# Optimization experiments

Measured on AMD Instinct MI355X. Metric: run time of the kernel, lower is better.

The kernel has to match this reference:

```python
import jax, jax.numpy as jnp
import numpy as np
from jax import lax

V, E, H, B, P, Q = 50000, 300, 256, 32, 400, 40


def _cell(x, h, c, Wih, Whh, b):
    # torch nn.LSTMCell math (b = b_ih + b_hh), gate order i,f,g,o
    g = x @ Wih.T + h @ Whh.T + b
    i, f, gg, o = jnp.split(g, 4, axis=-1)
    c2 = jax.nn.sigmoid(f) * c + jax.nn.sigmoid(i) * jnp.tanh(gg)
    return jax.nn.sigmoid(o) * jnp.tanh(c2), c2


def setup_inputs():
    key = jax.random.key(0)
    ks = jax.random.split(key, 26)
    n = lambda k, s: jax.random.normal(k, s, jnp.float32) * 0.05
    return {
        "passage_ids": jax.random.randint(ks[0], (P, B), 0, V),
        "question_ids": jax.random.randint(ks[1], (Q, B), 0, V),
        "passage_lens": jax.random.randint(ks[2], (B,), P // 2, P + 1),
        "question_lens": jax.random.randint(ks[3], (B,), Q // 2, Q + 1),
        "answer": jax.random.randint(ks[4], (2, B), 0, P // 2),
        "embed": n(ks[5], (V, E)),
        "pre_Wih": n(ks[6], (4 * H, E)),
        "pre_Whh": n(ks[7], (4 * H, H)),
        "pre_b": n(ks[8], (4 * H,)),
        "Wq": n(ks[9], (H, H)),
        "Wp": n(ks[10], (H, H)),
        "bp": n(ks[11], (H,)),
        "Wh": n(ks[12], (H, H)),
        "w_alpha": n(ks[13], (H,)),
        "b_alpha": n(ks[14], ()),
        "m_Wih": n(ks[15], (4 * H, 2 * H)),
        "m_Whh": n(ks[16], (4 * H, H)),
        "m_b": n(ks[17], (4 * H,)),
        "Wm": n(ks[18], (2 * H, H)),
        "Wa": n(ks[19], (H, H)),
        "ba": n(ks[20], (H,)),
        "w_beta": n(ks[21], (H,)),
        "b_beta": n(ks[22], ()),
        "p_Wih": n(ks[23], (4 * H, 2 * H)),
        "p_Whh": n(ks[24], (4 * H, H)),
        "p_b": n(ks[25], (4 * H,)),
    }


def _forward(embed, pre_Wih, pre_Whh, pre_b, Wq, Wp, bp, Wh, w_alpha, b_alpha,
             m_Wih, m_Whh, m_b, Wm, Wa, ba, w_beta, b_beta, p_Wih, p_Whh, p_b,
             passage_ids, passage_lens, question_ids, question_lens):
    Hd = pre_Whh.shape[1]
    Bd = passage_ids.shape[1]
    z0 = jnp.zeros((Bd, Hd), jnp.float32)

    def preprocess(ids, lens):
        x = embed[ids]                                       # [T,B,E]
        T = x.shape[0]
        m = (jnp.arange(T)[:, None] < lens[None, :]).astype(jnp.float32)[:, :, None]  # [T,B,1]
        def step(carry, inp):
            h, c = carry
            xt, mt = inp
            _, c2 = _cell(xt, h, c, pre_Wih, pre_Whh, pre_b)
            h2 = jnp.tanh(c2) * mt                           # module quirk: h := tanh(c)
            return (h2, c2 * mt), h2
        _, Hs = lax.scan(step, (z0, z0), (x, m))
        return Hs, m

    Hp, mP = preprocess(passage_ids, passage_lens)           # [P,B,H]
    Hq, _ = preprocess(question_ids, question_lens)          # [Q,B,H]

    attQ = Hq @ Wq                                           # [Q,B,H]

    def match(Hp_dir, m_dir):
        def step(carry, inp):
            h, c = carry
            hp, mt = inp                                     # hp [B,H], mt [B,1]
            g = jnp.tanh(attQ + hp @ Wp + bp + h @ Wh)       # [Q,B,H]
            alpha = jax.nn.softmax(g @ w_alpha + b_alpha, axis=0)  # softmax over question time [Q,B]
            wq = jnp.einsum('qb,qbh->bh', alpha, Hq)
            zt = jnp.concatenate([hp, wq], axis=-1) * mt
            h2, c2 = _cell(zt, h, c, m_Wih, m_Whh, m_b)
            h2 = h2 * mt
            return (h2, c2 * mt), h2
        _, Hs = lax.scan(step, (z0, z0), (Hp_dir, m_dir))
        return Hs

    Hf = match(Hp, mP)
    Hb = match(Hp[::-1], mP[::-1])[::-1]
    Hr = jnp.concatenate([Hf, Hb], axis=-1)                  # [P,B,2H]

    attM = Hr @ Wm                                           # [P,B,H]
    valid = (jnp.arange(Hr.shape[0])[:, None] < passage_lens[None, :]).astype(jnp.float32)  # [P,B]
    ha, ca = z0, z0
    dists = []
    for _ in range(2):                                       # start / end pointer
        Fk = jnp.tanh(attM + ha @ Wa + ba)                   # [P,B,H]
        scores = Fk @ w_beta + b_beta                        # [P,B]
        scores = jnp.where(valid > 0, scores, -1e30)
        beta = jax.nn.softmax(scores, axis=0) * valid        # zeros past passage length, like original
        dists.append(beta.T)                                 # [B,P]
        wHr = jnp.einsum('pb,pbh->bh', beta, Hr)
        ha, ca = _cell(wHr, ha, ca, p_Wih, p_Whh, p_b)
    return jnp.stack(dists)                                  # [2,B,P]


def reference(passage_ids, question_ids, passage_lens, question_lens, answer,
              embed, pre_Wih, pre_Whh, pre_b, Wq, Wp, bp, Wh, w_alpha, b_alpha,
              m_Wih, m_Whh, m_b, Wm, Wa, ba, w_beta, b_beta, p_Wih, p_Whh, p_b):
    # `answer` only feeds the training loss in the original; forward returns the distributions.
    return _forward(embed, pre_Wih, pre_Whh, pre_b, Wq, Wp, bp, Wh, w_alpha, b_alpha,
                    m_Wih, m_Whh, m_b, Wm, Wa, ba, w_beta, b_beta, p_Wih, p_Whh, p_b,
                    passage_ids, passage_lens, question_ids, question_lens)
```

## Files before the change

kernel.cpp:

```cpp
#include <hip/hip_runtime.h>
#include <hip/hip_bf16.h>

typedef __attribute__((ext_vector_type(8))) short short8;
typedef __attribute__((ext_vector_type(4))) float f32x4;
typedef __attribute__((ext_vector_type(2))) float f32x2;
typedef unsigned short u16;
typedef unsigned int u32;

#define DEV __device__ __forceinline__

static constexpr int Hd    = 256;
static constexpr int Bb    = 32;
static constexpr int Pp    = 400;
static constexpr int Qq    = 40;
static constexpr int NROWS = Pp * Bb + Qq * Bb;
static constexpr int PROBE_MAGIC = 1234567;
static constexpr int NPROBE = 14;

DEV float bf2f(u16 u) { u32 i = ((u32)u) << 16; float f; __builtin_memcpy(&f, &i, 4); return f; }
DEV u16 f2bf(float f) { u32 i; __builtin_memcpy(&i, &f, 4); i += 0x7FFFu + ((i >> 16) & 1u); return (u16)(i >> 16); }
DEV float sigf(float x) { return __builtin_amdgcn_rcpf(1.f + __expf(-x)); }
DEV float tanhf_(float x) {
  float ax = __builtin_fabsf(x);
  float t = __expf(2.f * ax);
  float r = 1.f - 2.f * __builtin_amdgcn_rcpf(t + 1.f);
  return x < 0.f ? -r : r;
}
DEV f32x4 mfma32(short8 a, short8 b, f32x4 c) {
  return __builtin_amdgcn_mfma_f32_16x16x32_bf16(a, b, c, 0, 0, 0);
}
DEV short8 zero8() { short8 z = {0,0,0,0,0,0,0,0}; return z; }

struct KArgs {
  const int *pids, *qids, *plen, *qlen;
  const float *embedF, *preWihF, *preWhhF, *preBF, *WqF, *WpF, *bpF, *WhF,
              *walphaF, *balphaF, *mWihF, *mWhhF, *mBF, *WmF, *WaF, *baF,
              *wbetaF, *bbetaF, *pWihF, *pWhhF, *pBF;
  int* bar;
  u16 *WqT, *WpT, *WmT, *WihP, *Xpad, *preX, *Hp, *Hq, *Hrb, *wq, *wHr, *haB,
      *attQb, *pWihB, *pWhhB, *mWxb, *WhTb, *xW;
  float *hpWp, *attM, *scores, *aWa, *gatesW;
  float* out;
};

DEV void probe_mark(int* bar, int idx) {
  if (blockIdx.x == 0 && threadIdx.x == 0)
    __hip_atomic_store(bar + 768 + idx, PROBE_MAGIC, __ATOMIC_RELEASE, __HIP_MEMORY_SCOPE_AGENT);
}

DEV void barn(int* base, int grp, int n, int gen) {
  __syncthreads();
  if (threadIdx.x == 0) {
    int* c = base + grp * 128;
    int* g = base + grp * 128 + 64;
    if (__hip_atomic_fetch_add(c, 1, __ATOMIC_ACQ_REL, __HIP_MEMORY_SCOPE_AGENT) == n - 1) {
      __hip_atomic_store(c, 0, __ATOMIC_RELAXED, __HIP_MEMORY_SCOPE_AGENT);
      __hip_atomic_store(g, gen, __ATOMIC_RELEASE, __HIP_MEMORY_SCOPE_AGENT);
    } else {
      while (__hip_atomic_load(g, __ATOMIC_RELAXED, __HIP_MEMORY_SCOPE_AGENT) < gen)
        __builtin_amdgcn_s_sleep(1);
      __builtin_amdgcn_fence(__ATOMIC_ACQUIRE, "agent");
    }
  }
  __syncthreads();
}

__global__ __launch_bounds__(256) void k_prep(KArgs A) {
  const int gtid = blockIdx.x * 256 + threadIdx.x;
  const int GS = 256 * 256;
  for (int idx = gtid; idx < 1024 * 160; idx += GS) {
    int row = idx / 160, cd = idx - row * 160;
    u32 v = 0;
    if (cd < 150) {
      f32x2 e2 = *(const f32x2*)(A.preWihF + (size_t)row * 300 + cd * 2);
      v = (u32)f2bf(e2[0]) | ((u32)f2bf(e2[1]) << 16);
    }
    *(u32*)(A.WihP + (size_t)row * 320 + cd * 2) = v;
  }
  for (int idx = gtid; idx < NROWS * 160; idx += GS) {
    int row = idx / 160, cd = idx - row * 160;
    int id = (row < Pp * Bb) ? A.pids[row] : A.qids[row - Pp * Bb];
    u32 v = 0;
    if (cd < 150) {
      f32x2 e2 = *(const f32x2*)(A.embedF + (size_t)id * 300 + cd * 2);
      v = (u32)f2bf(e2[0]) | ((u32)f2bf(e2[1]) << 16);
    }
    *(u32*)(A.Xpad + (size_t)row * 320 + cd * 2) = v;
  }
  for (int idx = gtid; idx < 65536; idx += GS) {
    int r = idx >> 8, c = idx & 255;
    A.WqT[idx]  = f2bf(A.WqF[c * 256 + r]);
    A.WpT[idx]  = f2bf(A.WpF[c * 256 + r]);
    A.WhTb[idx] = f2bf(A.WhF[c * 256 + r]);
  }
  for (int idx = gtid; idx < 131072; idx += GS) {
    int r = idx >> 9, c = idx & 511;
    A.WmT[idx] = f2bf(A.WmF[c * 256 + r]);
  }
  for (int idx = gtid; idx < 1024 * 256; idx += GS) {
    int n = idx >> 8, k = idx & 255;
    A.mWxb[idx] = f2bf(A.mWihF[(size_t)n * 512 + k]);
  }
  for (int idx = gtid; idx < 524288 + 262144; idx += GS) {
    if (idx < 524288) A.pWihB[idx] = f2bf(A.pWihF[idx]);
    else              A.pWhhB[idx - 524288] = f2bf(A.pWhhF[idx - 524288]);
  }
  if (gtid < 32 * 256) {
    A.aWa[gtid] = A.baF[gtid & 255];
    A.haB[gtid] = 0;
  }
  probe_mark(A.bar, 0);
}

struct GemmArgs { const u16* Ag; int lda; const u16* Bg; int ldb; int Mt64, Nt64, nk; float* Cf; u16* Cb; int ldc; int* bar; int probe; };

__global__ __launch_bounds__(512) void k_gemm(GemmArgs g) {
  const int tid = threadIdx.x, lane = tid & 63;
  const int r16 = lane & 15, kl = (lane >> 4) * 8;
  const int ntile = g.Mt64 * g.Nt64;
  const int stride = gridDim.x * 8;
  for (int tix = blockIdx.x * 8 + (tid >> 6); tix < ntile; tix += stride) {
    int m0 = (tix / g.Nt64) * 64, n0 = (tix % g.Nt64) * 64;
    f32x4 acc[4][4] = {};
    for (int kb = 0; kb < g.nk; ++kb) {
      int k0 = kb * 32 + kl;
      short8 a[4], b[4];
#pragma unroll
      for (int i = 0; i < 4; ++i) {
        a[i] = *(const short8*)(g.Ag + (size_t)(m0 + i * 16 + r16) * g.lda + k0);
        b[i] = *(const short8*)(g.Bg + (size_t)(n0 + i * 16 + r16) * g.ldb + k0);
      }
#pragma unroll
      for (int mi = 0; mi < 4; ++mi)
#pragma unroll
        for (int ni = 0; ni < 4; ++ni) acc[mi][ni] = mfma32(a[mi], b[ni], acc[mi][ni]);
    }
#pragma unroll
    for (int mi = 0; mi < 4; ++mi)
#pragma unroll
      for (int ni = 0; ni < 4; ++ni)
#pragma unroll
        for (int j = 0; j < 4; ++j) {
          int r = m0 + mi * 16 + (lane >> 4) * 4 + j, cc = n0 + ni * 16 + r16;
          if (g.Cf) g.Cf[(size_t)r * g.ldc + cc] = acc[mi][ni][j];
          else      g.Cb[(size_t)r * g.ldc + cc] = f2bf(acc[mi][ni][j]);
        }
  }
  probe_mark(g.bar, g.probe);
}

__global__ __launch_bounds__(512) void k_prescan(KArgs A) {
  __shared__ __align__(16) unsigned char sm[33280];
  float* PRE = (float*)(sm + 24576);
  float* CL  = (float*)(sm + 30720);
  float* PBL = (float*)(sm + 32768);
  const int blk = blockIdx.x;
  const int gi  = blk & 15;
  const int grp = blk >> 4;
  const int steps  = grp ? Qq : Pp;
  const int* lens  = grp ? A.qlen : A.plen;
  u16* Hs          = grp ? A.Hq : A.Hp;
  const int xoff   = grp ? Pp * Bb : 0;

  const int tid = threadIdx.x, lane = tid & 63, wv = tid >> 6;
  const int r16 = lane & 15, kl = (lane >> 4) * 8;
  const int h0 = gi * 16;

  for (int idx = tid; idx < 48 * 256; idx += 512) {
    int row = idx >> 8, k = idx & 255;
    int gate = (row >> 4) * 256 + h0 + (row & 15);
    int byte = row * 512 + ((2 * k) ^ ((row & 7) << 4));
    *(u16*)(sm + byte) = f2bf(A.preWhhF[(size_t)gate * 256 + k]);
  }
  for (int idx = tid; idx < 32 * 16; idx += 512) CL[idx] = 0.f;
  if (tid < 48) PBL[tid] = A.preBF[(tid >> 4) * 256 + h0 + (tid & 15)];
  __syncthreads();

  int gen = 0;
#pragma unroll 1
  for (int t = 0; t < steps; ++t) {
    if (wv < 6) {
      int mi = wv & 1, ni = wv >> 1;
      int chain = mi * 16 + r16;
      f32x4 acc = {0.f, 0.f, 0.f, 0.f};
#pragma unroll
      for (int kb = 0; kb < 8; ++kb) {
        int k0 = kb * 32 + kl;
        short8 a = zero8();
        if (t > 0) a = *(const short8*)(Hs + (size_t)((t - 1) * 32 + chain) * 256 + k0);
        int row = ni * 16 + r16;
        short8 b = *(const short8*)(sm + row * 512 + ((2 * k0) ^ ((row & 7) << 4)));
        acc = mfma32(a, b, acc);
      }
      int col = ni * 16 + r16;
#pragma unroll
      for (int j = 0; j < 4; ++j)
        PRE[(mi * 16 + (lane >> 4) * 4 + j) * 48 + col] = acc[j];
    }
    __syncthreads();
    {
      int chain = tid >> 4, hd = tid & 15;
      size_t xr = (size_t)(xoff + t * 32 + chain) * 1024;
      float ip = PRE[chain * 48 + hd]      + bf2f(A.preX[xr + h0 + hd])       + PBL[hd];
      float fp = PRE[chain * 48 + 16 + hd] + bf2f(A.preX[xr + 256 + h0 + hd]) + PBL[16 + hd];
      float gp = PRE[chain * 48 + 32 + hd] + bf2f(A.preX[xr + 512 + h0 + hd]) + PBL[32 + hd];
      float c2 = sigf(fp) * CL[chain * 16 + hd] + sigf(ip) * tanhf_(gp);
      float mt = (t < lens[chain]) ? 1.f : 0.f;
      float h2 = tanhf_(c2) * mt;
      c2 *= mt;
      CL[chain * 16 + hd] = c2;
      Hs[(size_t)(t * 32 + chain) * 256 + h0 + hd] = f2bf(h2);
    }
    barn(A.bar, grp, 16, ++gen);
  }
  probe_mark(A.bar, 2);
}

__global__ __launch_bounds__(512) void k_match(KArgs A) {
  __shared__ __align__(16) unsigned char sm[81920];
  float* PRE = (float*)(sm + 65536);
  float* CL  = (float*)(sm + 73728);
  float* EL  = (float*)(sm + 75776);
  float* SL  = (float*)(sm + 77824);
  float* AL  = (float*)(sm + 78336);
  float* BPL = (float*)(sm + 78848);
  float* WAL = (float*)(sm + 79872);
  float* MBL = (float*)(sm + 80896);

  const int blk = blockIdx.x;
  const int gi  = blk & 15;
  const int dir = blk >> 4;
  const int grp = 2 + dir;
  const int tid = threadIdx.x, lane = tid & 63, wv = tid >> 6;
  const int r16 = lane & 15, kl = (lane >> 4) * 8;
  const int h0 = gi * 16;

  for (int idx = tid; idx < 64 * 512; idx += 512) {
    int row = idx >> 9, k = idx & 511;
    int gate = (row >> 4) * 256 + h0 + (row & 15);
    float v = (k < 256) ? A.mWihF[(size_t)gate * 512 + 256 + k]
                        : A.mWhhF[(size_t)gate * 256 + (k - 256)];
    int byte = row * 1024 + ((2 * k) ^ ((row & 7) << 4));
    *(u16*)(sm + byte) = f2bf(v);
  }
  for (int idx = tid; idx < 32 * 16; idx += 512) CL[idx] = 0.f;
  if (tid < 256) { BPL[tid] = A.bpF[tid]; WAL[tid] = A.walphaF[tid]; }
  if (tid < 64) MBL[tid] = A.mBF[(tid >> 4) * 256 + h0 + (tid & 15)];
  __syncthreads();

  const float bAl = A.balphaF[0];
  int gen = 0;
#pragma unroll 1
  for (int t = 0; t < Pp; ++t) {
    int p  = dir ? (Pp - 1 - t) : t;
    int pp = dir ? (p + 1) : (p - 1);
    barn(A.bar, grp, 16, ++gen);

    if (t == 0) {
      EL[tid] = 0.f;
    } else {
      f32x4 acc0 = {0.f,0.f,0.f,0.f}, acc1 = {0.f,0.f,0.f,0.f};
#pragma unroll
      for (int kb = 0; kb < 8; ++kb) {
        int k0 = kb * 32 + kl;
        short8 a = zero8();
        if (r16 < 2)
          a = *(const short8*)(A.Hrb + (size_t)(pp * 32 + gi * 2 + r16) * 512 + dir * 256 + k0);
        short8 bA = *(const short8*)(A.WhTb + (size_t)(wv * 32 + r16) * 256 + k0);
        short8 bB = *(const short8*)(A.WhTb + (size_t)(wv * 32 + 16 + r16) * 256 + k0);
        acc0 = mfma32(a, bA, acc0);
        acc1 = mfma32(a, bB, acc1);
      }
      if ((lane >> 4) == 0) {
        EL[0 * 256 + wv * 32 + r16]      = acc0[0];
        EL[1 * 256 + wv * 32 + r16]      = acc0[1];
        EL[0 * 256 + wv * 32 + 16 + r16] = acc1[0];
        EL[1 * 256 + wv * 32 + 16 + r16] = acc1[1];
      }
    }
    __syncthreads();
    {
      int c = wv >> 2;
      int b = gi * 2 + c;
      float base[4];
#pragma unroll
      for (int j = 0; j < 4; ++j) {
        int h = lane + 64 * j;
        base[j] = A.hpWp[(size_t)(p * 32 + b) * 256 + h] + BPL[h] + EL[c * 256 + h];
      }
      int q4 = wv & 3;
#pragma unroll
      for (int i = 0; i < 10; ++i) {
        int q = q4 + 4 * i;
        float s = 0.f;
#pragma unroll
        for (int j = 0; j < 4; ++j) {
          int h = lane + 64 * j;
          s += WAL[h] * tanhf_(bf2f(A.attQb[(size_t)(q * 32 + b) * 256 + h]) + base[j]);
        }
#pragma unroll
        for (int off = 32; off; off >>= 1) s += __shfl_xor(s, off, 64);
        if (lane == 0) SL[c * 40 + q] = s;
      }
    }
    __syncthreads();
    if ((wv & 3) == 0) {
      int c = wv >> 2;
      float x = (lane < 40) ? (SL[c * 40 + lane] + bAl) : -3.4e38f;
      float m = x;
#pragma unroll
      for (int off = 32; off; off >>= 1) m = fmaxf(m, __shfl_xor(m, off, 64));
      float e = (lane < 40) ? __expf(x - m) : 0.f;
      float su = e;
#pragma unroll
      for (int off = 32; off; off >>= 1) su += __shfl_xor(su, off, 64);
      if (lane < 40) AL[c * 40 + lane] = e / su;
    }
    __syncthreads();
    {
      int c = tid >> 8, h = tid & 255;
      int b = gi * 2 + c;
      float acc = 0.f;
#pragma unroll 8
      for (int q = 0; q < 40; ++q) acc += AL[c * 40 + q] * bf2f(A.Hq[(size_t)(q * 32 + b) * 256 + h]);
      float mt = (p < A.plen[b]) ? 1.f : 0.f;
      A.wq[(size_t)(dir * 32 + b) * 256 + h] = f2bf(acc * mt);
    }
    barn(A.bar, grp, 16, ++gen);

    {
      int mi = wv >> 2, ni = wv & 3;
      int chain = mi * 16 + r16;
      f32x4 acc = {0.f, 0.f, 0.f, 0.f};
#pragma unroll
      for (int kb = 0; kb < 16; ++kb) {
        int k0 = kb * 32 + kl;
        short8 a;
        if (kb < 8) a = *(const short8*)(A.wq + (size_t)(dir * 32 + chain) * 256 + k0);
        else {
          if (t == 0) a = zero8();
          else        a = *(const short8*)(A.Hrb + (size_t)(pp * 32 + chain) * 512 + dir * 256 + (k0 - 256));
        }
        int row = ni * 16 + r16;
        short8 b = *(const short8*)(sm + row * 1024 + ((2 * k0) ^ ((row & 7) << 4)));
        acc = mfma32(a, b, acc);
      }
      int col = ni * 16 + r16;
#pragma unroll
      for (int j = 0; j < 4; ++j)
        PRE[(mi * 16 + (lane >> 4) * 4 + j) * 64 + col] = acc[j];
    }
    __syncthreads();
    {
      int chain = tid >> 4, hd = tid & 15;
      size_t xr = (size_t)(p * 32 + chain) * 1024 + h0 + hd;
      float ig = PRE[chain * 64 + hd]      + MBL[hd]      + bf2f(A.xW[xr]);
      float fg = PRE[chain * 64 + 16 + hd] + MBL[16 + hd] + bf2f(A.xW[xr + 256]);
      float gg = PRE[chain * 64 + 32 + hd] + MBL[32 + hd] + bf2f(A.xW[xr + 512]);
      float og = PRE[chain * 64 + 48 + hd] + MBL[48 + hd] + bf2f(A.xW[xr + 768]);
      float c2 = sigf(fg) * CL[chain * 16 + hd] + sigf(ig) * tanhf_(gg);
      float h2 = sigf(og) * tanhf_(c2);
      float mt = (p < A.plen[chain]) ? 1.f : 0.f;
      c2 *= mt; h2 *= mt;
      CL[chain * 16 + hd] = c2;
      A.Hrb[(size_t)(p * 32 + chain) * 512 + dir * 256 + h0 + hd] = f2bf(h2);
    }
  }
  probe_mark(A.bar, 6);
}

__global__ __launch_bounds__(512) void k_scores(KArgs A, int probe) {
  const int blk = blockIdx.x, tid = threadIdx.x, lane = tid & 63, wv = tid >> 6;
  for (int j = wv; j < 50; j += 8) {
    int id = blk * 50 + j;
    int p = id >> 5, b = id & 31;
    float s = 0.f;
#pragma unroll
    for (int jj = 0; jj < 4; ++jj) {
      int h = lane + 64 * jj;
      s += A.wbetaF[h] * tanhf_(A.attM[(size_t)(p * 32 + b) * 256 + h] + A.aWa[b * 256 + h]);
    }
#pragma unroll
    for (int off = 32; off; off >>= 1) s += __shfl_xor(s, off, 64);
    if (lane == 0)
      A.scores[p * 32 + b] = (p < A.plen[b]) ? (s + A.bbetaF[0]) : -1e30f;
  }
  probe_mark(A.bar, probe);
}

__global__ __launch_bounds__(512) void k_soft(KArgs A, int k, int probe) {
  __shared__ __align__(16) unsigned char sm[2048];
  float* BL = (float*)sm;
  float* RED = (float*)(sm + 1664);
  const int b = blockIdx.x, tid = threadIdx.x, lane = tid & 63, wv = tid >> 6;
  float x = (tid < 400) ? A.scores[tid * 32 + b] : -3.4e38f;
  float m = x;
#pragma unroll
  for (int off = 32; off; off >>= 1) m = fmaxf(m, __shfl_xor(m, off, 64));
  if (lane == 0) RED[wv] = m;
  __syncthreads();
  if (tid == 0) {
    float mm = RED[0];
#pragma unroll
    for (int i = 1; i < 8; ++i) mm = fmaxf(mm, RED[i]);
    RED[0] = mm;
  }
  __syncthreads();
  float M = RED[0];
  float e = (tid < 400) ? __expf(x - M) : 0.f;
  float su = e;
#pragma unroll
  for (int off = 32; off; off >>= 1) su += __shfl_xor(su, off, 64);
  if (lane == 0) RED[8 + wv] = su;
  __syncthreads();
  if (tid == 0) {
    float ss = 0.f;
#pragma unroll
    for (int i = 0; i < 8; ++i) ss += RED[8 + i];
    RED[8] = ss;
  }
  __syncthreads();
  float SUM = RED[8];
  if (tid < 400) {
    float beta = (e / SUM) * ((tid < A.plen[b]) ? 1.f : 0.f);
    A.out[(size_t)(k * 32 + b) * 400 + tid] = beta;
    BL[tid] = beta;
  }
  if (k == 0) {
    __syncthreads();
    float acc = 0.f;
#pragma unroll 4
    for (int p = 0; p < 400; ++p) acc += BL[p] * bf2f(A.Hrb[(size_t)(p * 32 + b) * 512 + tid]);
    A.wHr[b * 512 + tid] = f2bf(acc);
  }
  probe_mark(A.bar, probe);
}

__global__ __launch_bounds__(128) void k_pgates(KArgs A) {
  const int blk = blockIdx.x, tid = threadIdx.x, lane = tid & 63, wv = tid >> 6;
  const int r16 = lane & 15, kl = (lane >> 4) * 8;
  const int g0 = blk * 16;
  const int mi = wv, chain = mi * 16 + r16;
  f32x4 acc = {0.f, 0.f, 0.f, 0.f};
#pragma unroll
  for (int kb = 0; kb < 24; ++kb) {
    int k0 = kb * 32 + kl;
    short8 a, b;
    if (kb < 16) {
      a = *(const short8*)(A.wHr + (size_t)chain * 512 + k0);
      b = *(const short8*)(A.pWihB + (size_t)(g0 + r16) * 512 + k0);
    } else {
      a = *(const short8*)(A.haB + (size_t)chain * 256 + (k0 - 512));
      b = *(const short8*)(A.pWhhB + (size_t)(g0 + r16) * 256 + (k0 - 512));
    }
    acc = mfma32(a, b, acc);
  }
#pragma unroll
  for (int j = 0; j < 4; ++j)
    A.gatesW[(size_t)(mi * 16 + (lane >> 4) * 4 + j) * 1024 + g0 + r16] = acc[j];
  probe_mark(A.bar, 10);
}

__global__ __launch_bounds__(256) void k_pcell(KArgs A) {
  __shared__ float HL[256];
  const int b = blockIdx.x, hd = threadIdx.x;
  {
    float ig = A.gatesW[(size_t)b * 1024 + hd]       + A.pBF[hd];
    float gg = A.gatesW[(size_t)b * 1024 + 512 + hd] + A.pBF[512 + hd];
    float og = A.gatesW[(size_t)b * 1024 + 768 + hd] + A.pBF[768 + hd];
    float c2 = sigf(ig) * tanhf_(gg);
    float h2 = sigf(og) * tanhf_(c2);
    HL[hd] = h2;
    A.haB[b * 256 + hd] = f2bf(h2);
  }
  __syncthreads();
  {
    float acc = A.baF[hd];
#pragma unroll 8
    for (int kk = 0; kk < 256; ++kk) acc += HL[kk] * A.WaF[(size_t)kk * 256 + hd];
    A.aWa[b * 256 + hd] = acc;
  }
  probe_mark(A.bar, 11);
}

__global__ __launch_bounds__(64) void k_diag(KArgs A) {
  if (threadIdx.x == 0 && blockIdx.x == 0) {
    int bad = -1;
    for (int i = 0; i < NPROBE; ++i) {
      int v = __hip_atomic_load(A.bar + 768 + i, __ATOMIC_ACQUIRE, __HIP_MEMORY_SCOPE_AGENT);
      if (v != PROBE_MAGIC) { bad = i; break; }
    }
    if (bad >= 0) {
      float s = 128.f * (float)(1 << bad);
      for (int j = 0; j < 8; ++j) A.out[j] = s;
    }
  }
}

extern "C" void kernel_launch(void* const* d_in, const int* in_sizes, int n_in,
                              void* d_out, int out_size, void* d_ws, size_t ws_size,
                              hipStream_t stream) {
  (void)in_sizes; (void)n_in; (void)ws_size;
  KArgs A;
  A.pids = (const int*)d_in[0];
  A.qids = (const int*)d_in[1];
  A.plen = (const int*)d_in[2];
  A.qlen = (const int*)d_in[3];
  A.embedF  = (const float*)d_in[5];
  A.preWihF = (const float*)d_in[6];
  A.preWhhF = (const float*)d_in[7];
  A.preBF   = (const float*)d_in[8];
  A.WqF     = (const float*)d_in[9];
  A.WpF     = (const float*)d_in[10];
  A.bpF     = (const float*)d_in[11];
  A.WhF     = (const float*)d_in[12];
  A.walphaF = (const float*)d_in[13];
  A.balphaF = (const float*)d_in[14];
  A.mWihF   = (const float*)d_in[15];
  A.mWhhF   = (const float*)d_in[16];
  A.mBF     = (const float*)d_in[17];
  A.WmF     = (const float*)d_in[18];
  A.WaF     = (const float*)d_in[19];
  A.baF     = (const float*)d_in[20];
  A.wbetaF  = (const float*)d_in[21];
  A.bbetaF  = (const float*)d_in[22];
  A.pWihF   = (const float*)d_in[23];
  A.pWhhF   = (const float*)d_in[24];
  A.pBF     = (const float*)d_in[25];

  char* w = (char*)d_ws;
  size_t off = 0;
  auto take = [&](size_t bytes) { void* p = w + off; off += (bytes + 255) & ~(size_t)255; return p; };
  A.bar    = (int*)take(4096);
  A.WqT    = (u16*)take(256 * 256 * 2);
  A.WpT    = (u16*)take(256 * 256 * 2);
  A.WmT    = (u16*)take(256 * 512 * 2);
  A.WihP   = (u16*)take((size_t)1024 * 320 * 2);
  A.Xpad   = (u16*)take((size_t)NROWS * 320 * 2);
  A.preX   = (u16*)take((size_t)NROWS * 1024 * 2);
  A.Hp     = (u16*)take((size_t)Pp * Bb * 256 * 2);
  A.Hq     = (u16*)take((size_t)Qq * Bb * 256 * 2);
  A.Hrb    = (u16*)take((size_t)Pp * Bb * 512 * 2);
  A.wq     = (u16*)take(2 * 32 * 256 * 2);
  A.wHr    = (u16*)take(32 * 512 * 2);
  A.haB    = (u16*)take(32 * 256 * 2);
  A.attQb  = (u16*)take((size_t)Qq * Bb * 256 * 2);
  A.pWihB  = (u16*)take((size_t)1024 * 512 * 2);
  A.pWhhB  = (u16*)take((size_t)1024 * 256 * 2);
  A.mWxb   = (u16*)take((size_t)1024 * 256 * 2);
  A.WhTb   = (u16*)take((size_t)256 * 256 * 2);
  A.hpWp   = (float*)take((size_t)Pp * Bb * 256 * 4);
  A.attM   = (float*)take((size_t)Pp * Bb * 256 * 4);
  A.scores = (float*)take((size_t)Pp * Bb * 4);
  A.aWa    = (float*)take(32 * 256 * 4);
  A.gatesW = (float*)take((size_t)32 * 1024 * 4);
  A.xW     = A.preX;
  A.out    = (float*)d_out;

  hipMemsetAsync(d_out, 0x3C, 64, stream);
  hipMemsetAsync(A.bar, 0, 4096, stream);

  (void)hipGetLastError();
  size_t outB = (size_t)out_size * 4;
  int li = 0;
#define CK  if (hipGetLastError() != hipSuccess) { hipMemsetAsync(d_out, 0x41 + li, outB, stream); return; } ++li;

  hipLaunchKernelGGL(k_prep, dim3(256), dim3(256), 0, stream, A); CK;

  GemmArgs g1{A.Xpad, 320, A.WihP, 320, NROWS / 64, 16, 10, nullptr, A.preX, 1024, A.bar, 1};
  hipLaunchKernelGGL(k_gemm, dim3(256), dim3(512), 0, stream, g1); CK;

  hipLaunchKernelGGL(k_prescan, dim3(32), dim3(512), 0, stream, A); CK;

  GemmArgs g2{A.Hq, 256, A.WqT, 256, 20, 4, 8, nullptr, A.attQb, 256, A.bar, 3};
  hipLaunchKernelGGL(k_gemm, dim3(16), dim3(512), 0, stream, g2); CK;
  GemmArgs g3{A.Hp, 256, A.WpT, 256, 200, 4, 8, A.hpWp, nullptr, 256, A.bar, 4};
  hipLaunchKernelGGL(k_gemm, dim3(128), dim3(512), 0, stream, g3); CK;
  GemmArgs gx{A.Hp, 256, A.mWxb, 256, 200, 16, 8, nullptr, A.xW, 1024, A.bar, 5};
  hipLaunchKernelGGL(k_gemm, dim3(256), dim3(512), 0, stream, gx); CK;

  hipLaunchKernelGGL(k_match, dim3(32), dim3(512), 0, stream, A); CK;

  GemmArgs g4{A.Hrb, 512, A.WmT, 512, 200, 4, 16, A.attM, nullptr, 256, A.bar, 7};
  hipLaunchKernelGGL(k_gemm, dim3(128), dim3(512), 0, stream, g4); CK;

  hipLaunchKernelGGL(k_scores, dim3(256), dim3(512), 0, stream, A, 8); CK;
  hipLaunchKernelGGL(k_soft,   dim3(32),  dim3(512), 0, stream, A, 0, 9); CK;
  hipLaunchKernelGGL(k_pgates, dim3(64),  dim3(128), 0, stream, A); CK;
  hipLaunchKernelGGL(k_pcell,  dim3(32),  dim3(256), 0, stream, A); CK;
  hipLaunchKernelGGL(k_scores, dim3(256), dim3(512), 0, stream, A, 12); CK;
  hipLaunchKernelGGL(k_soft,   dim3(32),  dim3(512), 0, stream, A, 1, 13); CK;

  hipLaunchKernelGGL(k_diag,   dim3(1),   dim3(64),  0, stream, A); CK;
#undef CK
}
```

Before: 9.596 ms.

## Restructure match-LSTM step to prefetch inputs, split Wh projection, overlap GEMM with barrier

Each block now holds its 16-column slice of Wh in shared memory. After computing its h slice, it writes a partial h@Wh product to a per-block global buffer. At the next step the attention term sums the 16 partials instead of running a full 256x256 GEMM over the previous Hr row. Loop-invariant loads (attQ, hpWp, xW, Hq, preX) are hoisted ahead of the grid barrier, and the Hr half of the gate GEMM is issued before the barrier so it overlaps the wait. Global stores and loads of shared recurrent state switch to relaxed atomics with packed 32-bit stores, and the barrier acquire uses an atomic load. The cost is more register pressure, extra shared memory, and a bf16 rounding of each partial sum.

Result: slower. 14.73 ms (+53.5%).

```diff
diff --git a/kernel.cpp b/kernel.cpp
--- a/kernel.cpp
+++ b/kernel.cpp
@@ -6,6 +6,7 @@
 typedef __attribute__((ext_vector_type(2))) float f32x2;
 typedef unsigned short u16;
 typedef unsigned int u32;
+typedef unsigned long long u64;
 
 #define DEV __device__ __forceinline__
 
@@ -31,6 +32,22 @@
 }
 DEV short8 zero8() { short8 z = {0,0,0,0,0,0,0,0}; return z; }
 
+DEV void ast32(u32* p, u32 v) { __hip_atomic_store(p, v, __ATOMIC_RELAXED, __HIP_MEMORY_SCOPE_AGENT); }
+DEV u32 ald32(const u32* p) { return __hip_atomic_load(p, __ATOMIC_RELAXED, __HIP_MEMORY_SCOPE_AGENT); }
+DEV u64 ald64(const u64* p) { return __hip_atomic_load(p, __ATOMIC_RELAXED, __HIP_MEMORY_SCOPE_AGENT); }
+DEV short8 ald_frag(const u16* p) {
+  u64 q0 = ald64((const u64*)p);
+  u64 q1 = ald64((const u64*)(p + 4));
+  short8 v;
+  __builtin_memcpy(&v, &q0, 8);
+  __builtin_memcpy((char*)&v + 8, &q1, 8);
+  return v;
+}
+DEV u32 pack_pair(u16 mine, int lane) {
+  int other = __shfl_xor((int)mine, 1, 64);
+  return (lane & 1) ? 0u : ((u32)mine | ((u32)other << 16));
+}
+
 struct KArgs {
   const int *pids, *qids, *plen, *qlen;
   const float *embedF, *preWihF, *preWhhF, *preBF, *WqF, *WpF, *bpF, *WhF,
@@ -38,7 +55,7 @@
               *wbetaF, *bbetaF, *pWihF, *pWhhF, *pBF;
   int* bar;
   u16 *WqT, *WpT, *WmT, *WihP, *Xpad, *preX, *Hp, *Hq, *Hrb, *wq, *wHr, *haB,
-      *attQb, *pWihB, *pWhhB, *mWxb, *WhTb, *xW;
+      *attQb, *pWihB, *pWhhB, *mWxb, *xW, *peB;
   float *hpWp, *attM, *scores, *aWa, *gatesW;
   float* out;
 };
@@ -59,7 +76,7 @@
     } else {
       while (__hip_atomic_load(g, __ATOMIC_RELAXED, __HIP_MEMORY_SCOPE_AGENT) < gen)
         __builtin_amdgcn_s_sleep(1);
-      __builtin_amdgcn_fence(__ATOMIC_ACQUIRE, "agent");
+      (void)__hip_atomic_load(g, __ATOMIC_ACQUIRE, __HIP_MEMORY_SCOPE_AGENT);
     }
   }
   __syncthreads();
@@ -91,7 +108,6 @@
     int r = idx >> 8, c = idx & 255;
     A.WqT[idx]  = f2bf(A.WqF[c * 256 + r]);
     A.WpT[idx]  = f2bf(A.WpF[c * 256 + r]);
-    A.WhTb[idx] = f2bf(A.WhF[c * 256 + r]);
   }
   for (int idx = gtid; idx < 131072; idx += GS) {
     int r = idx >> 9, c = idx & 511;
@@ -176,9 +192,15 @@
   if (tid < 48) PBL[tid] = A.preBF[(tid >> 4) * 256 + h0 + (tid & 15)];
   __syncthreads();
 
+  const int chainC = tid >> 4, hd = tid & 15;
   int gen = 0;
 #pragma unroll 1
   for (int t = 0; t < steps; ++t) {
+    size_t xr = (size_t)(xoff + t * 32 + chainC) * 1024 + h0 + hd;
+    float xp0 = bf2f(A.preX[xr]);
+    float xp1 = bf2f(A.preX[xr + 256]);
+    float xp2 = bf2f(A.preX[xr + 512]);
+
     if (wv < 6) {
       int mi = wv & 1, ni = wv >> 1;
       int chain = mi * 16 + r16;
@@ -187,7 +209,7 @@
       for (int kb = 0; kb < 8; ++kb) {
         int k0 = kb * 32 + kl;
         short8 a = zero8();
-        if (t > 0) a = *(const short8*)(Hs + (size_t)((t - 1) * 32 + chain) * 256 + k0);
+        if (t > 0) a = ald_frag(Hs + (size_t)((t - 1) * 32 + chain) * 256 + k0);
         int row = ni * 16 + r16;
         short8 b = *(const short8*)(sm + row * 512 + ((2 * k0) ^ ((row & 7) << 4)));
         acc = mfma32(a, b, acc);
@@ -199,17 +221,18 @@
     }
     __syncthreads();
     {
-      int chain = tid >> 4, hd = tid & 15;
-      size_t xr = (size_t)(xoff + t * 32 + chain) * 1024;
-      float ip = PRE[chain * 48 + hd]      + bf2f(A.preX[xr + h0 + hd])       + PBL[hd];
-      float fp = PRE[chain * 48 + 16 + hd] + bf2f(A.preX[xr + 256 + h0 + hd]) + PBL[16 + hd];
-      float gp = PRE[chain * 48 + 32 + hd] + bf2f(A.preX[xr + 512 + h0 + hd]) + PBL[32 + hd];
-      float c2 = sigf(fp) * CL[chain * 16 + hd] + sigf(ip) * tanhf_(gp);
-      float mt = (t < lens[chain]) ? 1.f : 0.f;
+      float ip = PRE[chainC * 48 + hd]      + xp0 + PBL[hd];
+      float fp = PRE[chainC * 48 + 16 + hd] + xp1 + PBL[16 + hd];
+      float gp = PRE[chainC * 48 + 32 + hd] + xp2 + PBL[32 + hd];
+      float c2 = sigf(fp) * CL[chainC * 16 + hd] + sigf(ip) * tanhf_(gp);
+      float mt = (t < lens[chainC]) ? 1.f : 0.f;
       float h2 = tanhf_(c2) * mt;
       c2 *= mt;
-      CL[chain * 16 + hd] = c2;
-      Hs[(size_t)(t * 32 + chain) * 256 + h0 + hd] = f2bf(h2);
+      CL[chainC * 16 + hd] = c2;
+      u16 hb = f2bf(h2);
+      u32 pk = pack_pair(hb, lane);
+      if (!(lane & 1))
+        ast32((u32*)(Hs + (size_t)(t * 32 + chainC) * 256 + h0 + hd), pk);
     }
     barn(A.bar, grp, 16, ++gen);
   }
@@ -217,15 +240,17 @@
 }
 
 __global__ __launch_bounds__(512) void k_match(KArgs A) {
-  __shared__ __align__(16) unsigned char sm[81920];
-  float* PRE = (float*)(sm + 65536);
-  float* CL  = (float*)(sm + 73728);
-  float* EL  = (float*)(sm + 75776);
-  float* SL  = (float*)(sm + 77824);
-  float* AL  = (float*)(sm + 78336);
-  float* BPL = (float*)(sm + 78848);
-  float* WAL = (float*)(sm + 79872);
-  float* MBL = (float*)(sm + 80896);
+  __shared__ __align__(16) unsigned char sm[90112];
+  u16*   WHT = (u16*)(sm + 65536);
+  float* PRE = (float*)(sm + 73728);
+  float* CL  = (float*)(sm + 81920);
+  float* EL  = (float*)(sm + 83968);
+  u16*   H2L = (u16*)(sm + 86016);
+  float* SL  = (float*)(sm + 87040);
+  float* AL  = (float*)(sm + 87360);
+  float* BPL = (float*)(sm + 87680);
+  float* WAL = (float*)(sm + 88704);
+  float* MBL = (float*)(sm + 89728);
 
   const int blk = blockIdx.x;
   const int gi  = blk & 15;
@@ -234,6 +259,7 @@
   const int tid = threadIdx.x, lane = tid & 63, wv = tid >> 6;
   const int r16 = lane & 15, kl = (lane >> 4) * 8;
   const int h0 = gi * 16;
+  u16* peMine = A.peB + (size_t)((dir * 16 + gi) * 32) * 256;
 
   for (int idx = tid; idx < 64 * 512; idx += 512) {
     int row = idx >> 9, k = idx & 511;
@@ -243,52 +269,62 @@
     int byte = row * 1024 + ((2 * k) ^ ((row & 7) << 4));
     *(u16*)(sm + byte) = f2bf(v);
   }
+  for (int idx = tid; idx < 256 * 16; idx += 512) {
+    int h = idx >> 4, jj = idx & 15;
+    WHT[h * 16 + jj] = f2bf(A.WhF[(size_t)(h0 + jj) * 256 + h]);
+  }
   for (int idx = tid; idx < 32 * 16; idx += 512) CL[idx] = 0.f;
+  for (int idx = tid; idx < 32 * 128; idx += 512)
+    ast32((u32*)peMine + idx, 0u);
   if (tid < 256) { BPL[tid] = A.bpF[tid]; WAL[tid] = A.walphaF[tid]; }
   if (tid < 64) MBL[tid] = A.mBF[(tid >> 4) * 256 + h0 + (tid & 15)];
   __syncthreads();
 
   const float bAl = A.balphaF[0];
+  const int cS = wv >> 2, bS = gi * 2 + cS, q4 = wv & 3;
+  const int cW = tid >> 8, hW = tid & 255, bW = gi * 2 + cW;
+  const int chainC = tid >> 4, hd = tid & 15;
+  const int miG = wv >> 2, niG = wv & 3, chainG = miG * 16 + r16, rowG = niG * 16 + r16;
+
   int gen = 0;
 #pragma unroll 1
   for (int t = 0; t < Pp; ++t) {
     int p  = dir ? (Pp - 1 - t) : t;
     int pp = dir ? (p + 1) : (p - 1);
+
+    float aq[10][4], hw[4], xw4[4], hqv[40];
+#pragma unroll
+    for (int i = 0; i < 10; ++i)
+#pragma unroll
+      for (int j = 0; j < 4; ++j)
+        aq[i][j] = bf2f(A.attQb[(size_t)((q4 + 4 * i) * 32 + bS) * 256 + lane + 64 * j]);
+#pragma unroll
+    for (int j = 0; j < 4; ++j)
+      hw[j] = A.hpWp[(size_t)(p * 32 + bS) * 256 + lane + 64 * j];
+#pragma unroll
+    for (int g = 0; g < 4; ++g)
+      xw4[g] = bf2f(A.xW[(size_t)(p * 32 + chainC) * 1024 + g * 256 + h0 + hd]);
+#pragma unroll
+    for (int q = 0; q < 40; ++q)
+      hqv[q] = bf2f(A.Hq[(size_t)(q * 32 + bW) * 256 + hW]);
+
     barn(A.bar, grp, 16, ++gen);
 
-    if (t == 0) {
-      EL[tid] = 0.f;
-    } else {
-      f32x4 acc0 = {0.f,0.f,0.f,0.f}, acc1 = {0.f,0.f,0.f,0.f};
-#pragma unroll
-      for (int kb = 0; kb < 8; ++kb) {
-        int k0 = kb * 32 + kl;
-        short8 a = zero8();
-        if (r16 < 2)
-          a = *(const short8*)(A.Hrb + (size_t)(pp * 32 + gi * 2 + r16) * 512 + dir * 256 + k0);
-        short8 bA = *(const short8*)(A.WhTb + (size_t)(wv * 32 + r16) * 256 + k0);
-        short8 bB = *(const short8*)(A.WhTb + (size_t)(wv * 32 + 16 + r16) * 256 + k0);
-        acc0 = mfma32(a, bA, acc0);
-        acc1 = mfma32(a, bB, acc1);
+    if (tid < 256) {
+      int c = tid >> 7, h2 = tid & 127;
+      int b = gi * 2 + c;
+      float s0 = 0.f, s1 = 0.f;
+#pragma unroll
+      for (int g = 0; g < 16; ++g) {
+        u32 w = ald32((const u32*)(A.peB + (size_t)((dir * 16 + g) * 32 + b) * 256 + h2 * 2));
+        s0 += bf2f((u16)w);
+        s1 += bf2f((u16)(w >> 16));
       }
-      if ((lane >> 4) == 0) {
-        EL[0 * 256 + wv * 32 + r16]      = acc0[0];
-        EL[1 * 256 + wv * 32 + r16]      = acc0[1];
-        EL[0 * 256 + wv * 32 + 16 + r16] = acc1[0];
-        EL[1 * 256 + wv * 32 + 16 + r16] = acc1[1];
-      }
+      EL[c * 256 + h2 * 2]     = s0;
+      EL[c * 256 + h2 * 2 + 1] = s1;
     }
     __syncthreads();
     {
-      int c = wv >> 2;
-      int b = gi * 2 + c;
-      float base[4];
-#pragma unroll
-      for (int j = 0; j < 4; ++j) {
-        int h = lane + 64 * j;
-        base[j] = A.hpWp[(size_t)(p * 32 + b) * 256 + h] + BPL[h] + EL[c * 256 + h];
-      }
-      int q4 = wv & 3;
 #pragma unroll
       for (int i = 0; i < 10; ++i) {
         int q = q4 + 4 * i;
@@ -296,11 +332,11 @@
 #pragma unroll
         for (int j = 0; j < 4; ++j) {
           int h = lane + 64 * j;
-          s += WAL[h] * tanhf_(bf2f(A.attQb[(size_t)(q * 32 + b) * 256 + h]) + base[j]);
+          s += WAL[h] * tanhf_(aq[i][j] + hw[j] + BPL[h] + EL[cS * 256 + h]);
         }
 #pragma unroll
         for (int off = 32; off; off >>= 1) s += __shfl_xor(s, off, 64);
-        if (lane == 0) SL[c * 40 + q] = s;
+        if (lane == 0) SL[cS * 40 + q] = s;
       }
     }
     __syncthreads();
@@ -318,52 +354,80 @@
     }
     __syncthreads();
     {
-      int c = tid >> 8, h = tid & 255;
-      int b = gi * 2 + c;
       float acc = 0.f;
 #pragma unroll 8
-      for (int q = 0; q < 40; ++q) acc += AL[c * 40 + q] * bf2f(A.Hq[(size_t)(q * 32 + b) * 256 + h]);
-      float mt = (p < A.plen[b]) ? 1.f : 0.f;
-      A.wq[(size_t)(dir * 32 + b) * 256 + h] = f2bf(acc * mt);
+      for (int q = 0; q < 40; ++q) acc += AL[cW * 40 + q] * hqv[q];
+      float mt = (p < A.plen[bW]) ? 1.f : 0.f;
+      u16 wb = f2bf(acc * mt);
+      u32 pk = pack_pair(wb, lane);
+      if (!(lane & 1))
+        ast32((u32*)(A.wq + (size_t)(dir * 32 + bW) * 256 + hW), pk);
+    }
+    f32x4 accG = {0.f, 0.f, 0.f, 0.f};
+#pragma unroll
+    for (int kb = 8; kb < 16; ++kb) {
+      int k0 = kb * 32 + kl;
+      short8 a = zero8();
+      if (t > 0) a = ald_frag(A.Hrb + (size_t)(pp * 32 + chainG) * 512 + dir * 256 + (k0 - 256));
+      short8 b = *(const short8*)(sm + rowG * 1024 + ((2 * k0) ^ ((rowG & 7) << 4)));
+      accG = mfma32(a, b, accG);
     }
     barn(A.bar, grp, 16, ++gen);
 
+#pragma unroll
+    for (int kb = 0; kb < 8; ++kb) {
+      int k0 = kb * 32 + kl;
+      short8 a = ald_frag(A.wq + (size_t)(dir * 32 + chainG) * 256 + k0);
+      short8 b = *(const short8*)(sm + rowG * 1024 + ((2 * k0) ^ ((rowG & 7) << 4)));
+      accG = mfma32(a, b, accG);
+    }
     {
-      int mi = wv >> 2, ni = wv & 3;
-      int chain = mi * 16 + r16;
-      f32x4 acc = {0.f, 0.f, 0.f, 0.f};
-#pragma unroll
-      for (int kb = 0; kb < 16; ++kb) {
-        int k0 = kb * 32 + kl;
-        short8 a;
-        if (kb < 8) a = *(const short8*)(A.wq + (size_t)(dir * 32 + chain) * 256 + k0);
-        else {
-          if (t == 0) a = zero8();
-          else        a = *(const short8*)(A.Hrb + (size_t)(pp * 32 + chain) * 512 + dir * 256 + (k0 - 256));
-        }
-        int row = ni * 16 + r16;
-        short8 b = *(const short8*)(sm + row * 1024 + ((2 * k0) ^ ((row & 7) << 4)));
-        acc = mfma32(a, b, acc);
-      }
-      int col = ni * 16 + r16;
+      int col = niG * 16 + r16;
 #pragma unroll
       for (int j = 0; j < 4; ++j)
-        PRE[(mi * 16 + (lane >> 4) * 4 + j) * 64 + col] = acc[j];
+        PRE[(miG * 16 + (lane >> 4) * 4 + j) * 64 + col] = accG[j];
     }
     __syncthreads();
     {
-      int chain = tid >> 4, hd = tid & 15;
-      size_t xr = (size_t)(p * 32 + chain) * 1024 + h0 + hd;
-      float ig = PRE[chain * 64 + hd]      + MBL[hd]      + bf2f(A.xW[xr]);
-      float fg = PRE[chain * 64 + 16 + hd] + MBL[16 + hd] + bf2f(A.xW[xr + 256]);
-      float gg = PRE[chain * 64 + 32 + hd] + MBL[32 + hd] + bf2f(A.xW[xr + 512]);
-      float og = PRE[chain * 64 + 48 + hd] + MBL[48 + hd] + bf2f(A.xW[xr + 768]);
-      float c2 = sigf(fg) * CL[chain * 16 + hd] + sigf(ig) * tanhf_(gg);
+      float ig = PRE[chainC * 64 + hd]      + MBL[hd]      + xw4[0];
+      float fg = PRE[chainC * 64 + 16 + hd] + MBL[16 + hd] + xw4[1];
+      float gg = PRE[chainC * 64 + 32 + hd] + MBL[32 + hd] + xw4[2];
+      float og = PRE[chainC * 64 + 48 + hd] + MBL[48 + hd] + xw4[3];
+      float c2 = sigf(fg) * CL[chainC * 16 + hd] + sigf(ig) * tanhf_(gg);
       float h2 = sigf(og) * tanhf_(c2);
-      float mt = (p < A.plen[chain]) ? 1.f : 0.f;
+      float mt = (p < A.plen[chainC]) ? 1.f : 0.f;
       c2 *= mt; h2 *= mt;
-      CL[chain * 16 + hd] = c2;
-      A.Hrb[(size_t)(p * 32 + chain) * 512 + dir * 256 + h0 + hd] = f2bf(h2);
+      CL[chainC * 16 + hd] = c2;
+      u16 hb = f2bf(h2);
+      H2L[chainC * 16 + hd] = hb;
+      u32 pk = pack_pair(hb, lane);
+      if (!(lane & 1))
+        ast32((u32*)(A.Hrb + (size_t)(p * 32 + chainC) * 512 + dir * 256 + h0 + hd), pk);
+    }
+    __syncthreads();
+    {
+#pragma unroll
+      for (int i = 0; i < 4; ++i) {
+        int task = wv * 4 + i;
+        int nf = task & 15, mi = task >> 4;
+        int chain = mi * 16 + r16;
+        int hcol = nf * 16 + r16;
+        short8 a = zero8(), b = zero8();
+        if (kl < 16) {
+          a = *(const short8*)(H2L + chain * 16 + kl);
+          b = *(const short8*)(WHT + hcol * 16 + kl);
+        }
+        f32x4 acc = {0.f, 0.f, 0.f, 0.f};
+        acc = mfma32(a, b, acc);
+#pragma unroll
+        for (int j = 0; j < 4; ++j) {
+          u16 vb = f2bf(acc[j]);
+          u32 pk = pack_pair(vb, lane);
+          int row = mi * 16 + (lane >> 4) * 4 + j;
+          if (!(lane & 1))
+            ast32((u32*)(peMine + (size_t)row * 256 + hcol), pk);
+        }
+      }
     }
   }
   probe_mark(A.bar, 6);
@@ -548,7 +612,7 @@
   A.pWihB  = (u16*)take((size_t)1024 * 512 * 2);
   A.pWhhB  = (u16*)take((size_t)1024 * 256 * 2);
   A.mWxb   = (u16*)take((size_t)1024 * 256 * 2);
-  A.WhTb   = (u16*)take((size_t)256 * 256 * 2);
+  A.peB    = (u16*)take((size_t)2 * 16 * 32 * 256 * 2);
   A.hpWp   = (float*)take((size_t)Pp * Bb * 256 * 4);
   A.attM   = (float*)take((size_t)Pp * Bb * 256 * 4);
   A.scores = (float*)take((size_t)Pp * Bb * 4);
```
